# Performance work log

Measured on AMD Instinct MI355X. Metric: run time of the kernel, lower is better.

## Reference

```python
import jax, jax.numpy as jnp
import numpy as np

B, SRC_LEN, IN_DIM = 4096, 128, 16
H = 64
SEQ_LEN = 100
MEAN_DIM = 4
COV_DIM = MEAN_DIM + MEAN_DIM * (MEAN_DIM - 1) // 2  # 10
SKIP = 4


def _lin_init(key, out_d, in_d):
    k1, k2 = jax.random.split(key)
    bound = 1.0 / np.sqrt(in_d)
    W = jax.random.uniform(k1, (out_d, in_d), minval=-bound, maxval=bound, dtype=jnp.float32)
    b = jax.random.uniform(k2, (out_d,), minval=-bound, maxval=bound, dtype=jnp.float32)
    return W, b


def setup_inputs() -> dict:
    key = jax.random.key(0)
    ks = jax.random.split(key, 16)
    inp = {}
    inp["x"] = jax.random.normal(ks[0], (B, SRC_LEN, IN_DIM), dtype=jnp.float32)
    inp["trg"] = jax.random.normal(ks[1], (B, 1, SKIP), dtype=jnp.float32)
    # encoder GRU (1 layer)
    inp["enc_Wih"], inp["enc_bih"] = _lin_init(ks[2], 3 * H, IN_DIM)
    inp["enc_Whh"], inp["enc_bhh"] = _lin_init(ks[3], 3 * H, H)
    # decoder GRU (1 layer)
    inp["dec_Wih"], inp["dec_bih"] = _lin_init(ks[4], 3 * H, IN_DIM)
    inp["dec_Whh"], inp["dec_bhh"] = _lin_init(ks[5], 3 * H, H)
    # decoder.out: Linear(H -> IN_DIM)
    inp["out_W"], inp["out_b"] = _lin_init(ks[6], IN_DIM, H)
    # initEmbed: Linear(SKIP -> IN_DIM)
    inp["emb_W"], inp["emb_b"] = _lin_init(ks[7], IN_DIM, SKIP)
    # mean head: Linear(IN_DIM->H), GELU, Linear(H->MEAN_DIM)
    inp["mh_W1"], inp["mh_b1"] = _lin_init(ks[8], H, IN_DIM)
    inp["mh_W2"], inp["mh_b2"] = _lin_init(ks[9], MEAN_DIM, H)
    # cov head: Linear(IN_DIM->H), GELU, Linear(H->COV_DIM)
    inp["ch_W1"], inp["ch_b1"] = _lin_init(ks[10], H, IN_DIM)
    inp["ch_W2"], inp["ch_b2"] = _lin_init(ks[11], COV_DIM, H)
    return inp


def _gru_cell(h, xt, Wih, Whh, bih, bhh):
    # PyTorch GRU cell math. h, xt: [B, H], [B, in]
    gi = xt @ Wih.T + bih           # [B, 3H]
    gh = h @ Whh.T + bhh            # [B, 3H]
    i_r, i_z, i_n = jnp.split(gi, 3, axis=-1)
    h_r, h_z, h_n = jnp.split(gh, 3, axis=-1)
    r = jax.nn.sigmoid(i_r + h_r)
    z = jax.nn.sigmoid(i_z + h_z)
    n = jnp.tanh(i_n + r * h_n)
    return (1.0 - z) * n + z * h


def reference(x, trg, enc_Wih, enc_bih, enc_Whh, enc_bhh,
              dec_Wih, dec_bih, dec_Whh, dec_bhh,
              out_W, out_b, emb_W, emb_b,
              mh_W1, mh_b1, mh_W2, mh_b2,
              ch_W1, ch_b1, ch_W2, ch_b2):
    b = x.shape[0]
    # ---- encoder GRU over src_len; only final hidden is used downstream ----
    h0 = jnp.zeros((b, H), dtype=x.dtype)

    def enc_step(h, xt):
        h = _gru_cell(h, xt, enc_Wih, enc_Whh, enc_bih, enc_bhh)
        return h, None

    enc_h, _ = jax.lax.scan(enc_step, h0, jnp.swapaxes(x, 0, 1))

    init_in = trg[:, 0, :] @ emb_W.T + emb_b  # [B, IN_DIM]

    def dec_step(carry, _):
        h, inp = carry
        h = _gru_cell(h, inp, dec_Wih, dec_Whh, dec_bih, dec_bhh)
        o = h @ out_W.T + out_b               # [B, IN_DIM]
        nxt = jax.lax.stop_gradient(o)        # .detach() on fed-back input
        return (h, nxt), o

    (_, _), outs = jax.lax.scan(dec_step, (enc_h, init_in), None, length=SEQ_LEN)
    dec_out = jnp.swapaxes(outs, 0, 1)        # [B, SEQ_LEN, IN_DIM]

    # ---- output heads (Dropout is identity in eval) ----
    means = jax.nn.gelu(dec_out @ mh_W1.T + mh_b1, approximate=False) @ mh_W2.T + mh_b2
    covs = jax.nn.gelu(dec_out @ ch_W1.T + ch_b1, approximate=False) @ ch_W2.T + ch_b2

    inf = jnp.inf
    lower = jnp.array([-inf, -inf, -1.0, -1.0], dtype=means.dtype)
    upper = jnp.array([inf, inf, 1.0, 1.0], dtype=means.dtype)
    means = jnp.maximum(jnp.minimum(means, upper), lower)
    return means, covs
```

## Files before the change

### kernel.cpp

```cpp
#include <hip/hip_runtime.h>
#include <cstdint>
#include <cstddef>

#define BTOT    4096
#define SRCLEN  128
#define INDIM   16
#define HDIM    64
#define SEQLEN  100
#define MEANS_N (BTOT * SEQLEN * 4)

__device__ __forceinline__ float sigmoidf_(float x) {
    return __builtin_amdgcn_rcpf(1.0f + __expf(-x));
}
__device__ __forceinline__ float tanhf_(float x) {
    float e = __expf(2.0f * x);
    return 1.0f - 2.0f * __builtin_amdgcn_rcpf(e + 1.0f);
}
__device__ __forceinline__ float gelu_fast(float x) {
    float z = fabsf(x) * 0.70710678118654752440f;
    float t = __builtin_amdgcn_rcpf(1.0f + 0.3275911f * z);
    float p = t * (0.254829592f +
              t * (-0.284496736f +
              t * (1.421413741f +
              t * (-1.453152027f +
              t * 1.061405429f))));
    float er = 1.0f - p * __expf(-z * z);
    er = copysignf(er, x);
    return 0.5f * x * (1.0f + er);
}

typedef __attribute__((ext_vector_type(8))) short s8v;
typedef __attribute__((ext_vector_type(4))) float f4v;

__device__ __forceinline__ unsigned short f2bf(float x) {
    unsigned u = __float_as_uint(x);
    unsigned r = (u + 0x7FFFu + ((u >> 16) & 1u)) >> 16;
    return (unsigned short)r;
}
__device__ __forceinline__ float bf2f(unsigned short b) {
    return __uint_as_float(((unsigned)b) << 16);
}
__device__ __forceinline__ void split2(float4 a, float4 b, s8v& hi, s8v& lo) {
    float v[8] = {a.x, a.y, a.z, a.w, b.x, b.y, b.z, b.w};
    #pragma unroll
    for (int j = 0; j < 8; ++j) {
        unsigned short h = f2bf(v[j]);
        hi[j] = (short)h;
        lo[j] = (short)f2bf(v[j] - bf2f(h));
    }
}
__device__ __forceinline__ void split8(const float* v, s8v& hi, s8v& lo) {
    #pragma unroll
    for (int j = 0; j < 8; ++j) {
        unsigned short h = f2bf(v[j]);
        hi[j] = (short)h;
        lo[j] = (short)f2bf(v[j] - bf2f(h));
    }
}
__device__ __forceinline__ void load_bfrag(const float* p, s8v& hi, s8v& lo) {
    float4 a = *(const float4*)p;
    float4 b = *(const float4*)(p + 4);
    split2(a, b, hi, lo);
}

typedef __attribute__((ext_vector_type(2))) unsigned int u2v;
__device__ __forceinline__ float half_merge(float own_lo, float send_hi) {
    u2v r = __builtin_amdgcn_permlane32_swap(__float_as_uint(own_lo),
                                             __float_as_uint(send_hi),
                                             false, false);
    return __uint_as_float(r[0]);
}

#define MFMA16(a, b, c) __builtin_amdgcn_mfma_f32_16x16x32_bf16((a), (b), (c), 0, 0, 0)

__global__ __launch_bounds__(256, 2) void fused_gru_kernel(
    const float* __restrict__ x,
    const float* __restrict__ eWih, const float* __restrict__ ebih,
    const float* __restrict__ eWhh, const float* __restrict__ ebhh,
    const float* __restrict__ dWih, const float* __restrict__ dbih,
    const float* __restrict__ dWhh, const float* __restrict__ dbhh,
    const float* __restrict__ outW, const float* __restrict__ outb,
    const float* __restrict__ embW, const float* __restrict__ embb,
    const float* __restrict__ trg,
    float* __restrict__ dec_o)
{
    const int tid  = threadIdx.x;
    const int lane = tid & 63;
    const int w    = tid >> 6;
    const int col  = lane & 15;
    const int q    = lane >> 4;
    const int u    = w * 16 + col;
    const int b0   = blockIdx.x * 8;
    const int rj0  = (q & 1) * 4 + ((q >> 1) << 1);

    __shared__ __align__(16) unsigned short hiL[2][16][72];
    __shared__ __align__(16) unsigned short loL[2][16][72];
    __shared__ __align__(16) unsigned short xhi_l[64][9][16];
    __shared__ __align__(16) unsigned short xlo_l[64][9][16];
    __shared__ float outW_l[16][64];
    __shared__ float init_l[8][16];

    for (int i = tid; i < 16 * 64; i += 256) outW_l[i >> 6][i & 63] = outW[i];
    if (tid < 128) {
        int b = tid >> 4, jj = tid & 15;
        float s = embb[jj];
        #pragma unroll
        for (int s4 = 0; s4 < 4; ++s4)
            s = fmaf(embW[jj * 4 + s4], trg[(size_t)(b0 + b) * 4 + s4], s);
        init_l[b][jj] = s;
    }

    for (int i = tid; i < 2 * 16 * 72; i += 256) {
        ((unsigned short*)hiL)[i] = 0;
        ((unsigned short*)loL)[i] = 0;
    }
    for (int i = tid; i < 64 * 16; i += 256) {
        xhi_l[i >> 4][8][i & 15] = 0;
        xlo_l[i >> 4][8][i & 15] = 0;
    }

    auto stage_x = [&](int c) {
        #pragma unroll
        for (int k = 0; k < 8; ++k) {
            int f   = tid + k * 256;
            int b   = f >> 8;
            int rem = f & 255;
            int tl  = rem >> 2;
            int d4  = (rem & 3) << 2;
            const float* xp = x + ((size_t)(b0 + b) * SRCLEN + (c * 64 + tl)) * INDIM + d4;
            float4 v = *(const float4*)xp;
            float vv[4] = {v.x, v.y, v.z, v.w};
            unsigned short hh[4], ll[4];
            #pragma unroll
            for (int j = 0; j < 4; ++j) {
                hh[j] = f2bf(vv[j]);
                ll[j] = f2bf(vv[j] - bf2f(hh[j]));
            }
            *(ushort4*)&xhi_l[tl][b][d4] = make_ushort4(hh[0], hh[1], hh[2], hh[3]);
            *(ushort4*)&xlo_l[tl][b][d4] = make_ushort4(ll[0], ll[1], ll[2], ll[3]);
        }
    };

    const s8v z8 = {0, 0, 0, 0, 0, 0, 0, 0};
    const f4v z4 = {0.0f, 0.0f, 0.0f, 0.0f};

    {
        s8v brh[3], brl[3], bzh[3], bzl[3], bnhh[2], bnhl[2], bnxh, bnxl;
        load_bfrag(eWhh + (size_t)u * 64 + q * 8,              brh[0], brl[0]);
        load_bfrag(eWhh + (size_t)u * 64 + 32 + q * 8,         brh[1], brl[1]);
        load_bfrag(eWhh + (size_t)(64 + u) * 64 + q * 8,       bzh[0], bzl[0]);
        load_bfrag(eWhh + (size_t)(64 + u) * 64 + 32 + q * 8,  bzh[1], bzl[1]);
        load_bfrag(eWhh + (size_t)(128 + u) * 64 + q * 8,      bnhh[0], bnhl[0]);
        load_bfrag(eWhh + (size_t)(128 + u) * 64 + 32 + q * 8, bnhh[1], bnhl[1]);
        if (q < 2) {
            load_bfrag(eWih + (size_t)u * 16 + q * 8,         brh[2], brl[2]);
            load_bfrag(eWih + (size_t)(64 + u) * 16 + q * 8,  bzh[2], bzl[2]);
            load_bfrag(eWih + (size_t)(128 + u) * 16 + q * 8, bnxh, bnxl);
        } else {
            brh[2] = z8; brl[2] = z8; bzh[2] = z8; bzl[2] = z8; bnxh = z8; bnxl = z8;
        }

        const float br   = ebih[u] + ebhh[u];
        const float bz   = ebih[u + 64] + ebhh[u + 64];
        const float bnx  = ebih[u + 128];
        const float bnh  = ebhh[u + 128];

        const int xb   = (q < 2) ? (col & 7) : 8;
        const int xoff = (q & 1) * 8;
        const unsigned short* xh_base = &xhi_l[0][xb][xoff];
        const unsigned short* xl_base = &xlo_l[0][xb][xoff];

        stage_x(0);
        float hold2e[2] = {0.0f, 0.0f};
        __syncthreads();

        int cur = 0;
        for (int t = 0; t < SRCLEN; ++t) {
            if (t == 64) {
                stage_x(1);
                __syncthreads();
            }
            const int tl = t & 63;

            const s8v xh = *(const s8v*)(xh_base + (size_t)tl * 144);
            const s8v xl = *(const s8v*)(xl_base + (size_t)tl * 144);

            const s8v ah0 = *(const s8v*)&hiL[cur][col][q * 8];
            const s8v al0 = *(const s8v*)&loL[cur][col][q * 8];
            const s8v ah1 = *(const s8v*)&hiL[cur][col][32 + q * 8];
            const s8v al1 = *(const s8v*)&loL[cur][col][32 + q * 8];

            f4v accr, accz, accnh, accnx;
            accr  = MFMA16(ah0, brh[0], z4);
            accz  = MFMA16(ah0, bzh[0], z4);
            accnh = MFMA16(ah0, bnhh[0], z4);
            accr  = MFMA16(ah0, brl[0], accr);
            accz  = MFMA16(ah0, bzl[0], accz);
            accnh = MFMA16(ah0, bnhl[0], accnh);
            accr  = MFMA16(al0, brh[0], accr);
            accz  = MFMA16(al0, bzh[0], accz);
            accnh = MFMA16(al0, bnhh[0], accnh);
            accr  = MFMA16(ah1, brh[1], accr);
            accz  = MFMA16(ah1, bzh[1], accz);
            accnh = MFMA16(ah1, bnhh[1], accnh);
            accr  = MFMA16(ah1, brl[1], accr);
            accz  = MFMA16(ah1, bzl[1], accz);
            accnh = MFMA16(ah1, bnhl[1], accnh);
            accr  = MFMA16(al1, brh[1], accr);
            accz  = MFMA16(al1, bzh[1], accz);
            accnh = MFMA16(al1, bnhh[1], accnh);
            accr  = MFMA16(xh, brh[2], accr);
            accz  = MFMA16(xh, bzh[2], accz);
            accnx = MFMA16(xh, bnxh, z4);
            accr  = MFMA16(xh, brl[2], accr);
            accz  = MFMA16(xh, bzl[2], accz);
            accnx = MFMA16(xh, bnxl, accnx);
            accr  = MFMA16(xl, brh[2], accr);
            accz  = MFMA16(xl, bzh[2], accz);
            accnx = MFMA16(xl, bnxh, accnx);

            float pr[2], pz[2], pnh[2], pnx[2];
            pr[0]  = half_merge(accr[0],  accr[2]);
            pr[1]  = half_merge(accr[1],  accr[3]);
            pz[0]  = half_merge(accz[0],  accz[2]);
            pz[1]  = half_merge(accz[1],  accz[3]);
            pnh[0] = half_merge(accnh[0], accnh[2]);
            pnh[1] = half_merge(accnh[1], accnh[3]);
            pnx[0] = half_merge(accnx[0], accnx[2]);
            pnx[1] = half_merge(accnx[1], accnx[3]);

            const int nxt = cur ^ 1;
            #pragma unroll
            for (int j = 0; j < 2; ++j) {
                float r  = sigmoidf_(pr[j] + br);
                float zz = sigmoidf_(pz[j] + bz);
                float n  = tanhf_(pnx[j] + bnx + r * (pnh[j] + bnh));
                float h  = (1.0f - zz) * n + zz * hold2e[j];
                hold2e[j] = h;
                unsigned short hh = f2bf(h);
                hiL[nxt][rj0 + j][u] = hh;
                loL[nxt][rj0 + j][u] = f2bf(h - bf2f(hh));
            }
            __syncthreads();
            cur ^= 1;
        }

        float hold2[2] = {hold2e[0], hold2e[1]};

        float wh_r[16], wh_z[16], wh_n[16];
        #pragma unroll
        for (int c = 0; c < 2; ++c)
            #pragma unroll
            for (int jj = 0; jj < 8; ++jj) {
                int k = c * 32 + q * 8 + jj;
                wh_r[c * 8 + jj] = dWhh[(size_t)u * 64 + k];
                wh_z[c * 8 + jj] = dWhh[(size_t)(64 + u) * 64 + k];
                wh_n[c * 8 + jj] = dWhh[(size_t)(128 + u) * 64 + k];
            }
        float wi_r[16], wi_z[16], wi_n[16];
        #pragma unroll
        for (int j = 0; j < 16; ++j) {
            wi_r[j] = dWih[(size_t)u * 16 + j];
            wi_z[j] = dWih[(size_t)(64 + u) * 16 + j];
            wi_n[j] = dWih[(size_t)(128 + u) * 16 + j];
        }

        float m_r[16], m_z[16], c_in[16];
        #pragma unroll
        for (int c = 0; c < 2; ++c)
            #pragma unroll
            for (int jj = 0; jj < 8; ++jj) {
                int k = c * 32 + q * 8 + jj;
                float sr = 0.0f, sz = 0.0f, sn = 0.0f;
                #pragma unroll
                for (int j = 0; j < 16; ++j) {
                    float ow = outW_l[j][k];
                    sr = fmaf(wi_r[j], ow, sr);
                    sz = fmaf(wi_z[j], ow, sz);
                    sn = fmaf(wi_n[j], ow, sn);
                }
                m_r[c * 8 + jj]  = wh_r[c * 8 + jj] + sr;
                m_z[c * 8 + jj]  = wh_z[c * 8 + jj] + sz;
                c_in[c * 8 + jj] = sn;
            }

        s8v mrh[2], mrl[2], mzh[2], mzl[2], cinh[2], cinl[2], hnh[2], hnl[2];
        split8(m_r,      mrh[0],  mrl[0]);  split8(m_r + 8,  mrh[1],  mrl[1]);
        split8(m_z,      mzh[0],  mzl[0]);  split8(m_z + 8,  mzh[1],  mzl[1]);
        split8(c_in,     cinh[0], cinl[0]); split8(c_in + 8, cinh[1], cinl[1]);
        split8(wh_n,     hnh[0],  hnl[0]);  split8(wh_n + 8, hnh[1],  hnl[1]);
        s8v r0h[2], r0l[2], z0h[2], z0l[2];
        split8(wh_r, r0h[0], r0l[0]); split8(wh_r + 8, r0h[1], r0l[1]);
        split8(wh_z, z0h[0], z0l[0]); split8(wh_z + 8, z0h[1], z0l[1]);
        s8v owh[2], owl[2];
        {
            float ov[16];
            #pragma unroll
            for (int c = 0; c < 2; ++c)
                #pragma unroll
                for (int jj = 0; jj < 8; ++jj)
                    ov[c * 8 + jj] = outW_l[col][c * 32 + q * 8 + jj];
            split8(ov, owh[0], owl[0]); split8(ov + 8, owh[1], owl[1]);
        }

        float b_r = dbhh[u] + dbih[u];
        float b_z = dbhh[u + 64] + dbih[u + 64];
        float b_in = dbih[u + 128];
        const float b_hn = dbhh[u + 128];
        #pragma unroll
        for (int j = 0; j < 16; ++j) {
            float obj = outb[j];
            b_r  = fmaf(obj, wi_r[j], b_r);
            b_z  = fmaf(obj, wi_z[j], b_z);
            b_in = fmaf(obj, wi_n[j], b_in);
        }
        const float ob = outb[col];

        float g_r[2], g_z[2], g_n[2];
        #pragma unroll
        for (int j2 = 0; j2 < 2; ++j2) {
            int row = rj0 + j2;
            float sr = dbih[u] + dbhh[u];
            float sz = dbih[u + 64] + dbhh[u + 64];
            float sn = dbih[u + 128];
            #pragma unroll
            for (int j = 0; j < 16; ++j) {
                float iv = init_l[row][j];
                sr = fmaf(wi_r[j], iv, sr);
                sz = fmaf(wi_z[j], iv, sz);
                sn = fmaf(wi_n[j], iv, sn);
            }
            g_r[j2] = sr; g_z[j2] = sz; g_n[j2] = sn;
        }

        {
            const s8v ah0 = *(const s8v*)&hiL[0][col][q * 8];
            const s8v al0 = *(const s8v*)&loL[0][col][q * 8];
            const s8v ah1 = *(const s8v*)&hiL[0][col][32 + q * 8];
            const s8v al1 = *(const s8v*)&loL[0][col][32 + q * 8];
            f4v ar, az, ahn;
            ar  = MFMA16(ah0, r0h[0], z4);
            az  = MFMA16(ah0, z0h[0], z4);
            ahn = MFMA16(ah0, hnh[0], z4);
            ar  = MFMA16(ah0, r0l[0], ar);
            az  = MFMA16(ah0, z0l[0], az);
            ahn = MFMA16(ah0, hnl[0], ahn);
            ar  = MFMA16(al0, r0h[0], ar);
            az  = MFMA16(al0, z0h[0], az);
            ahn = MFMA16(al0, hnh[0], ahn);
            ar  = MFMA16(ah1, r0h[1], ar);
            az  = MFMA16(ah1, z0h[1], az);
            ahn = MFMA16(ah1, hnh[1], ahn);
            ar  = MFMA16(ah1, r0l[1], ar);
            az  = MFMA16(ah1, z0l[1], az);
            ahn = MFMA16(ah1, hnl[1], ahn);
            ar  = MFMA16(al1, r0h[1], ar);
            az  = MFMA16(al1, z0h[1], az);
            ahn = MFMA16(al1, hnh[1], ahn);

            float pr[2], pz[2], pnh[2];
            pr[0]  = half_merge(ar[0],  ar[2]);
            pr[1]  = half_merge(ar[1],  ar[3]);
            pz[0]  = half_merge(az[0],  az[2]);
            pz[1]  = half_merge(az[1],  az[3]);
            pnh[0] = half_merge(ahn[0], ahn[2]);
            pnh[1] = half_merge(ahn[1], ahn[3]);

            #pragma unroll
            for (int j = 0; j < 2; ++j) {
                float r  = sigmoidf_(pr[j] + g_r[j]);
                float zz = sigmoidf_(pz[j] + g_z[j]);
                float n  = tanhf_(g_n[j] + r * (pnh[j] + b_hn));
                float h  = (1.0f - zz) * n + zz * hold2[j];
                hold2[j] = h;
                unsigned short hh = f2bf(h);
                hiL[1][rj0 + j][u] = hh;
                loL[1][rj0 + j][u] = f2bf(h - bf2f(hh));
            }
            __syncthreads();
        }

        for (int t = 1; t < SEQLEN; ++t) {
            const int dcur = t & 1;
            const s8v ah0 = *(const s8v*)&hiL[dcur][col][q * 8];
            const s8v al0 = *(const s8v*)&loL[dcur][col][q * 8];
            const s8v ah1 = *(const s8v*)&hiL[dcur][col][32 + q * 8];
            const s8v al1 = *(const s8v*)&loL[dcur][col][32 + q * 8];

            if (w == ((t - 1) & 3)) {
                f4v oa;
                oa = MFMA16(ah0, owh[0], z4);
                oa = MFMA16(ah0, owl[0], oa);
                oa = MFMA16(al0, owh[0], oa);
                oa = MFMA16(ah1, owh[1], oa);
                oa = MFMA16(ah1, owl[1], oa);
                oa = MFMA16(al1, owh[1], oa);
                if (q < 2) {
                    #pragma unroll
                    for (int i = 0; i < 4; ++i)
                        dec_o[(((size_t)(b0 + q * 4 + i) * SEQLEN) + (t - 1)) * INDIM + col] = oa[i] + ob;
                }
            }

            f4v ar, az, ain, ahn;
            ar  = MFMA16(ah0, mrh[0], z4);
            az  = MFMA16(ah0, mzh[0], z4);
            ain = MFMA16(ah0, cinh[0], z4);
            ahn = MFMA16(ah0, hnh[0], z4);
            ar  = MFMA16(ah0, mrl[0], ar);
            az  = MFMA16(ah0, mzl[0], az);
            ain = MFMA16(ah0, cinl[0], ain);
            ahn = MFMA16(ah0, hnl[0], ahn);
            ar  = MFMA16(al0, mrh[0], ar);
            az  = MFMA16(al0, mzh[0], az);
            ain = MFMA16(al0, cinh[0], ain);
            ahn = MFMA16(al0, hnh[0], ahn);
            ar  = MFMA16(ah1, mrh[1], ar);
            az  = MFMA16(ah1, mzh[1], az);
            ain = MFMA16(ah1, cinh[1], ain);
            ahn = MFMA16(ah1, hnh[1], ahn);
            ar  = MFMA16(ah1, mrl[1], ar);
            az  = MFMA16(ah1, mzl[1], az);
            ain = MFMA16(ah1, cinl[1], ain);
            ahn = MFMA16(ah1, hnl[1], ahn);
            ar  = MFMA16(al1, mrh[1], ar);
            az  = MFMA16(al1, mzh[1], az);
            ain = MFMA16(al1, cinh[1], ain);
            ahn = MFMA16(al1, hnh[1], ahn);

            float pr[2], pz[2], pin[2], pnh[2];
            pr[0]  = half_merge(ar[0],  ar[2]);
            pr[1]  = half_merge(ar[1],  ar[3]);
            pz[0]  = half_merge(az[0],  az[2]);
            pz[1]  = half_merge(az[1],  az[3]);
            pin[0] = half_merge(ain[0], ain[2]);
            pin[1] = half_merge(ain[1], ain[3]);
            pnh[0] = half_merge(ahn[0], ahn[2]);
            pnh[1] = half_merge(ahn[1], ahn[3]);

            const int nxt = dcur ^ 1;
            #pragma unroll
            for (int j = 0; j < 2; ++j) {
                float r  = sigmoidf_(pr[j] + b_r);
                float zz = sigmoidf_(pz[j] + b_z);
                float n  = tanhf_(pin[j] + b_in + r * (pnh[j] + b_hn));
                float h  = (1.0f - zz) * n + zz * hold2[j];
                hold2[j] = h;
                unsigned short hh = f2bf(h);
                hiL[nxt][rj0 + j][u] = hh;
                loL[nxt][rj0 + j][u] = f2bf(h - bf2f(hh));
            }
            __syncthreads();
        }

        if (w == 0) {
            const s8v ah0 = *(const s8v*)&hiL[0][col][q * 8];
            const s8v al0 = *(const s8v*)&loL[0][col][q * 8];
            const s8v ah1 = *(const s8v*)&hiL[0][col][32 + q * 8];
            const s8v al1 = *(const s8v*)&loL[0][col][32 + q * 8];
            f4v oa;
            oa = MFMA16(ah0, owh[0], z4);
            oa = MFMA16(ah0, owl[0], oa);
            oa = MFMA16(al0, owh[0], oa);
            oa = MFMA16(ah1, owh[1], oa);
            oa = MFMA16(ah1, owl[1], oa);
            oa = MFMA16(al1, owh[1], oa);
            if (q < 2) {
                #pragma unroll
                for (int i = 0; i < 4; ++i)
                    dec_o[(((size_t)(b0 + q * 4 + i) * SEQLEN) + (SEQLEN - 1)) * INDIM + col] = oa[i] + ob;
            }
        }
    }
}

__global__ __launch_bounds__(256) void heads_mfma_kernel(
    const float* __restrict__ dec_o,
    const float* __restrict__ mW1, const float* __restrict__ mb1,
    const float* __restrict__ mW2, const float* __restrict__ mb2,
    const float* __restrict__ cW1, const float* __restrict__ cb1,
    const float* __restrict__ cW2, const float* __restrict__ cb2,
    float* __restrict__ out)
{
    const int tid  = threadIdx.x;
    const int lane = tid & 63;
    const int w    = tid >> 6;
    const int col  = lane & 15;
    const int q    = lane >> 4;

    __shared__ __align__(16) unsigned short Hm_hi[4][16][72];
    __shared__ __align__(16) unsigned short Hm_lo[4][16][72];
    __shared__ __align__(16) unsigned short Hc_hi[4][16][72];
    __shared__ __align__(16) unsigned short Hc_lo[4][16][72];

    const s8v z8 = {0, 0, 0, 0, 0, 0, 0, 0};
    const f4v z4 = {0.0f, 0.0f, 0.0f, 0.0f};

    s8v w1mh[4], w1ml[4], w1ch[4], w1cl[4];
    #pragma unroll
    for (int c = 0; c < 4; ++c) {
        if (q < 2) {
            load_bfrag(mW1 + (size_t)(c * 16 + col) * 16 + q * 8, w1mh[c], w1ml[c]);
            load_bfrag(cW1 + (size_t)(c * 16 + col) * 16 + q * 8, w1ch[c], w1cl[c]);
        } else {
            w1mh[c] = z8; w1ml[c] = z8; w1ch[c] = z8; w1cl[c] = z8;
        }
    }
    s8v w2mh[2], w2ml[2], w2ch[2], w2cl[2];
    if (col < 4) {
        load_bfrag(mW2 + (size_t)col * 64 + q * 8,      w2mh[0], w2ml[0]);
        load_bfrag(mW2 + (size_t)col * 64 + 32 + q * 8, w2mh[1], w2ml[1]);
    } else {
        w2mh[0] = z8; w2ml[0] = z8; w2mh[1] = z8; w2ml[1] = z8;
    }
    if (col < 10) {
        load_bfrag(cW2 + (size_t)col * 64 + q * 8,      w2ch[0], w2cl[0]);
        load_bfrag(cW2 + (size_t)col * 64 + 32 + q * 8, w2ch[1], w2cl[1]);
    } else {
        w2ch[0] = z8; w2cl[0] = z8; w2ch[1] = z8; w2cl[1] = z8;
    }

    float b1m[4], b1c[4];
    #pragma unroll
    for (int c = 0; c < 4; ++c) {
        b1m[c] = mb1[c * 16 + col];
        b1c[c] = cb1[c * 16 + col];
    }
    const float b2m = (col < 4)  ? mb2[col] : 0.0f;
    const float b2c = (col < 10) ? cb2[col] : 0.0f;

    float* means = out;
    float* covs  = out + MEANS_N;

    const int wave_id = blockIdx.x * 4 + w;

    #pragma unroll 1
    for (int it = 0; it < 4; ++it) {
        const int tile = wave_id + 6400 * it;
        const size_t r0 = (size_t)tile * 16;

        s8v ah, al;
        if (q < 2) {
            load_bfrag(dec_o + (r0 + (size_t)col) * 16 + q * 8, ah, al);
        } else { ah = z8; al = z8; }

        #pragma unroll
        for (int c = 0; c < 4; ++c) {
            f4v am = MFMA16(ah, w1mh[c], z4);
            am = MFMA16(ah, w1ml[c], am);
            am = MFMA16(al, w1mh[c], am);
            f4v ac = MFMA16(ah, w1ch[c], z4);
            ac = MFMA16(ah, w1cl[c], ac);
            ac = MFMA16(al, w1ch[c], ac);
            #pragma unroll
            for (int i = 0; i < 4; ++i) {
                float hm = gelu_fast(am[i] + b1m[c]);
                unsigned short hh = f2bf(hm);
                Hm_hi[w][q * 4 + i][c * 16 + col] = hh;
                Hm_lo[w][q * 4 + i][c * 16 + col] = f2bf(hm - bf2f(hh));
                float hc = gelu_fast(ac[i] + b1c[c]);
                hh = f2bf(hc);
                Hc_hi[w][q * 4 + i][c * 16 + col] = hh;
                Hc_lo[w][q * 4 + i][c * 16 + col] = f2bf(hc - bf2f(hh));
            }
        }

        const s8v amh0 = *(const s8v*)&Hm_hi[w][col][q * 8];
        const s8v amh1 = *(const s8v*)&Hm_hi[w][col][32 + q * 8];
        const s8v aml0 = *(const s8v*)&Hm_lo[w][col][q * 8];
        const s8v aml1 = *(const s8v*)&Hm_lo[w][col][32 + q * 8];
        const s8v ach0 = *(const s8v*)&Hc_hi[w][col][q * 8];
        const s8v ach1 = *(const s8v*)&Hc_hi[w][col][32 + q * 8];
        const s8v acl0 = *(const s8v*)&Hc_lo[w][col][q * 8];
        const s8v acl1 = *(const s8v*)&Hc_lo[w][col][32 + q * 8];

        f4v om, oc;
        om = MFMA16(amh0, w2mh[0], z4);
        om = MFMA16(amh0, w2ml[0], om);
        om = MFMA16(aml0, w2mh[0], om);
        om = MFMA16(amh1, w2mh[1], om);
        om = MFMA16(amh1, w2ml[1], om);
        om = MFMA16(aml1, w2mh[1], om);
        oc = MFMA16(ach0, w2ch[0], z4);
        oc = MFMA16(ach0, w2cl[0], oc);
        oc = MFMA16(acl0, w2ch[0], oc);
        oc = MFMA16(ach1, w2ch[1], oc);
        oc = MFMA16(ach1, w2cl[1], oc);
        oc = MFMA16(acl1, w2ch[1], oc);

        if (col < 4) {
            #pragma unroll
            for (int i = 0; i < 4; ++i) {
                float v = om[i] + b2m;
                if (col >= 2) v = fminf(fmaxf(v, -1.0f), 1.0f);
                means[(r0 + q * 4 + i) * 4 + col] = v;
            }
        }
        if (col < 10) {
            #pragma unroll
            for (int i = 0; i < 4; ++i)
                covs[(r0 + q * 4 + i) * 10 + col] = oc[i] + b2c;
        }
    }
}

extern "C" void kernel_launch(void* const* d_in, const int* in_sizes, int n_in,
                              void* d_out, int out_size, void* d_ws, size_t ws_size,
                              hipStream_t stream)
{
    const float* x    = (const float*)d_in[0];
    const float* trg  = (const float*)d_in[1];
    const float* eWih = (const float*)d_in[2];
    const float* ebih = (const float*)d_in[3];
    const float* eWhh = (const float*)d_in[4];
    const float* ebhh = (const float*)d_in[5];
    const float* dWih = (const float*)d_in[6];
    const float* dbih = (const float*)d_in[7];
    const float* dWhh = (const float*)d_in[8];
    const float* dbhh = (const float*)d_in[9];
    const float* outW = (const float*)d_in[10];
    const float* outb = (const float*)d_in[11];
    const float* embW = (const float*)d_in[12];
    const float* embb = (const float*)d_in[13];
    const float* mW1  = (const float*)d_in[14];
    const float* mb1  = (const float*)d_in[15];
    const float* mW2  = (const float*)d_in[16];
    const float* mb2  = (const float*)d_in[17];
    const float* cW1  = (const float*)d_in[18];
    const float* cb1  = (const float*)d_in[19];
    const float* cW2  = (const float*)d_in[20];
    const float* cb2  = (const float*)d_in[21];

    float* ws    = (float*)d_ws;
    float* dec_o = ws;
    float* outp  = (float*)d_out;

    fused_gru_kernel<<<dim3(BTOT / 8), dim3(256), 0, stream>>>(
        x, eWih, ebih, eWhh, ebhh, dWih, dbih, dWhh, dbhh,
        outW, outb, embW, embb, trg, dec_o);
    heads_mfma_kernel<<<dim3(1600), dim3(256), 0, stream>>>(
        dec_o, mW1, mb1, mW2, mb2, cW1, cb1, cW2, cb2, outp);
}
```

Before: 349.0 us.

## Fuse output heads into decoder loop as a software-pipelined stage

Removes the separate heads kernel and the dec_o workspace round trip. The heads now run inside the decoder time loop: the per-step output goes to shared memory, layer 1 of both heads runs one step later, and layer 2 runs two steps later on waves 2 and 3. This saves a kernel launch and the global write and read of the decoder outputs, hiding head work in the latency-bound recurrence. In exchange it adds MFMA and GELU work, two extra loop iterations, and more shared memory and registers in a kernel launched with launch_bounds(256,2).

After: 477.3 us. 36.8% more time.

```diff
diff --git a/kernel.cpp b/kernel.cpp
--- a/kernel.cpp
+++ b/kernel.cpp
@@ -82,7 +82,11 @@
     const float* __restrict__ outW, const float* __restrict__ outb,
     const float* __restrict__ embW, const float* __restrict__ embb,
     const float* __restrict__ trg,
-    float* __restrict__ dec_o)
+    const float* __restrict__ mW1, const float* __restrict__ mb1,
+    const float* __restrict__ mW2, const float* __restrict__ mb2,
+    const float* __restrict__ cW1, const float* __restrict__ cb1,
+    const float* __restrict__ cW2, const float* __restrict__ cb2,
+    float* __restrict__ out)
 {
     const int tid  = threadIdx.x;
     const int lane = tid & 63;
@@ -99,6 +103,11 @@
     __shared__ __align__(16) unsigned short xlo_l[64][9][16];
     __shared__ float outW_l[16][64];
     __shared__ float init_l[8][16];
+    __shared__ __align__(16) float o_sl[2][8][16];
+    __shared__ __align__(16) unsigned short Hm_hi[2][8][72];
+    __shared__ __align__(16) unsigned short Hm_lo[2][8][72];
+    __shared__ __align__(16) unsigned short Hc_hi[2][8][72];
+    __shared__ __align__(16) unsigned short Hc_lo[2][8][72];
 
     for (int i = tid; i < 16 * 64; i += 256) outW_l[i >> 6][i & 63] = outW[i];
     if (tid < 128) {
@@ -144,6 +153,7 @@
     const s8v z8 = {0, 0, 0, 0, 0, 0, 0, 0};
     const f4v z4 = {0.0f, 0.0f, 0.0f, 0.0f};
 
+    float hold2e[2];
     {
         s8v brh[3], brl[3], bzh[3], bzl[3], bnhh[2], bnhl[2], bnxh, bnxl;
         load_bfrag(eWhh + (size_t)u * 64 + q * 8,              brh[0], brl[0]);
@@ -171,7 +181,7 @@
         const unsigned short* xl_base = &xlo_l[0][xb][xoff];
 
         stage_x(0);
-        float hold2e[2] = {0.0f, 0.0f};
+        hold2e[0] = 0.0f; hold2e[1] = 0.0f;
         __syncthreads();
 
         int cur = 0;
@@ -244,7 +254,9 @@
             __syncthreads();
             cur ^= 1;
         }
-
+    }
+
+    {
         float hold2[2] = {hold2e[0], hold2e[1]};
 
         float wh_r[16], wh_z[16], wh_n[16];
@@ -315,6 +327,33 @@
             b_in = fmaf(obj, wi_n[j], b_in);
         }
         const float ob = outb[col];
+
+        s8v w1mh, w1ml, w1ch, w1cl;
+        if (q < 2) {
+            load_bfrag(mW1 + (size_t)(w * 16 + col) * 16 + q * 8, w1mh, w1ml);
+            load_bfrag(cW1 + (size_t)(w * 16 + col) * 16 + q * 8, w1ch, w1cl);
+        } else { w1mh = z8; w1ml = z8; w1ch = z8; w1cl = z8; }
+        const float b1m = mb1[w * 16 + col];
+        const float b1c = cb1[w * 16 + col];
+        s8v w2h[2], w2l[2];
+        w2h[0] = z8; w2l[0] = z8; w2h[1] = z8; w2l[1] = z8;
+        float b2 = 0.0f;
+        if (w == 2) {
+            if (col < 4) {
+                load_bfrag(mW2 + (size_t)col * 64 + q * 8,      w2h[0], w2l[0]);
+                load_bfrag(mW2 + (size_t)col * 64 + 32 + q * 8, w2h[1], w2l[1]);
+                b2 = mb2[col];
+            }
+        } else if (w == 3) {
+            if (col < 10) {
+                load_bfrag(cW2 + (size_t)col * 64 + q * 8,      w2h[0], w2l[0]);
+                load_bfrag(cW2 + (size_t)col * 64 + 32 + q * 8, w2h[1], w2l[1]);
+                b2 = cb2[col];
+            }
+        }
+
+        float* means = out;
+        float* covs  = out + MEANS_N;
 
         float g_r[2], g_z[2], g_n[2];
         #pragma unroll
@@ -380,226 +419,161 @@
             __syncthreads();
         }
 
-        for (int t = 1; t < SEQLEN; ++t) {
+        for (int t = 1; t <= SEQLEN + 2; ++t) {
             const int dcur = t & 1;
-            const s8v ah0 = *(const s8v*)&hiL[dcur][col][q * 8];
-            const s8v al0 = *(const s8v*)&loL[dcur][col][q * 8];
-            const s8v ah1 = *(const s8v*)&hiL[dcur][col][32 + q * 8];
-            const s8v al1 = *(const s8v*)&loL[dcur][col][32 + q * 8];
-
-            if (w == ((t - 1) & 3)) {
-                f4v oa;
-                oa = MFMA16(ah0, owh[0], z4);
-                oa = MFMA16(ah0, owl[0], oa);
-                oa = MFMA16(al0, owh[0], oa);
-                oa = MFMA16(ah1, owh[1], oa);
-                oa = MFMA16(ah1, owl[1], oa);
-                oa = MFMA16(al1, owh[1], oa);
+
+            if (t <= SEQLEN) {
+                const s8v ah0 = *(const s8v*)&hiL[dcur][col][q * 8];
+                const s8v al0 = *(const s8v*)&loL[dcur][col][q * 8];
+                const s8v ah1 = *(const s8v*)&hiL[dcur][col][32 + q * 8];
+                const s8v al1 = *(const s8v*)&loL[dcur][col][32 + q * 8];
+
+                if (w == ((t - 1) & 3)) {
+                    f4v oa;
+                    oa = MFMA16(ah0, owh[0], z4);
+                    oa = MFMA16(ah0, owl[0], oa);
+                    oa = MFMA16(al0, owh[0], oa);
+                    oa = MFMA16(ah1, owh[1], oa);
+                    oa = MFMA16(ah1, owl[1], oa);
+                    oa = MFMA16(al1, owh[1], oa);
+                    if (q < 2) {
+                        #pragma unroll
+                        for (int i = 0; i < 4; ++i)
+                            o_sl[dcur][q * 4 + i][col] = oa[i] + ob;
+                    }
+                }
+
+                if (t < SEQLEN) {
+                    f4v ar, az, ain, ahn;
+                    ar  = MFMA16(ah0, mrh[0], z4);
+                    az  = MFMA16(ah0, mzh[0], z4);
+                    ain = MFMA16(ah0, cinh[0], z4);
+                    ahn = MFMA16(ah0, hnh[0], z4);
+                    ar  = MFMA16(ah0, mrl[0], ar);
+                    az  = MFMA16(ah0, mzl[0], az);
+                    ain = MFMA16(ah0, cinl[0], ain);
+                    ahn = MFMA16(ah0, hnl[0], ahn);
+                    ar  = MFMA16(al0, mrh[0], ar);
+                    az  = MFMA16(al0, mzh[0], az);
+                    ain = MFMA16(al0, cinh[0], ain);
+                    ahn = MFMA16(al0, hnh[0], ahn);
+                    ar  = MFMA16(ah1, mrh[1], ar);
+                    az  = MFMA16(ah1, mzh[1], az);
+                    ain = MFMA16(ah1, cinh[1], ain);
+                    ahn = MFMA16(ah1, hnh[1], ahn);
+                    ar  = MFMA16(ah1, mrl[1], ar);
+                    az  = MFMA16(ah1, mzl[1], az);
+                    ain = MFMA16(ah1, cinl[1], ain);
+                    ahn = MFMA16(ah1, hnl[1], ahn);
+                    ar  = MFMA16(al1, mrh[1], ar);
+                    az  = MFMA16(al1, mzh[1], az);
+                    ain = MFMA16(al1, cinh[1], ain);
+                    ahn = MFMA16(al1, hnh[1], ahn);
+
+                    float pr[2], pz[2], pin[2], pnh[2];
+                    pr[0]  = half_merge(ar[0],  ar[2]);
+                    pr[1]  = half_merge(ar[1],  ar[3]);
+                    pz[0]  = half_merge(az[0],  az[2]);
+                    pz[1]  = half_merge(az[1],  az[3]);
+                    pin[0] = half_merge(ain[0], ain[2]);
+                    pin[1] = half_merge(ain[1], ain[3]);
+                    pnh[0] = half_merge(ahn[0], ahn[2]);
+                    pnh[1] = half_merge(ahn[1], ahn[3]);
+
+                    const int nxt = dcur ^ 1;
+                    #pragma unroll
+                    for (int j = 0; j < 2; ++j) {
+                        float r  = sigmoidf_(pr[j] + b_r);
+                        float zz = sigmoidf_(pz[j] + b_z);
+                        float n  = tanhf_(pin[j] + b_in + r * (pnh[j] + b_hn));
+                        float h  = (1.0f - zz) * n + zz * hold2[j];
+                        hold2[j] = h;
+                        unsigned short hh = f2bf(h);
+                        hiL[nxt][rj0 + j][u] = hh;
+                        loL[nxt][rj0 + j][u] = f2bf(h - bf2f(hh));
+                    }
+                }
+            }
+
+            if (t >= 2) {
+                const int po = (t - 1) & 1;
+                const int ph = t & 1;
+                s8v aoh, aol;
+                if (q < 2 && col < 8) {
+                    float4 a = *(const float4*)&o_sl[po][col][q * 8];
+                    float4 b = *(const float4*)&o_sl[po][col][q * 8 + 4];
+                    split2(a, b, aoh, aol);
+                } else { aoh = z8; aol = z8; }
+
+                f4v am = MFMA16(aoh, w1mh, z4);
+                am = MFMA16(aoh, w1ml, am);
+                am = MFMA16(aol, w1mh, am);
+                f4v ac = MFMA16(aoh, w1ch, z4);
+                ac = MFMA16(aoh, w1cl, ac);
+                ac = MFMA16(aol, w1ch, ac);
+
                 if (q < 2) {
                     #pragma unroll
-                    for (int i = 0; i < 4; ++i)
-                        dec_o[(((size_t)(b0 + q * 4 + i) * SEQLEN) + (t - 1)) * INDIM + col] = oa[i] + ob;
+                    for (int i = 0; i < 4; ++i) {
+                        float hm = gelu_fast(am[i] + b1m);
+                        unsigned short hh = f2bf(hm);
+                        Hm_hi[ph][q * 4 + i][w * 16 + col] = hh;
+                        Hm_lo[ph][q * 4 + i][w * 16 + col] = f2bf(hm - bf2f(hh));
+                        float hc = gelu_fast(ac[i] + b1c);
+                        hh = f2bf(hc);
+                        Hc_hi[ph][q * 4 + i][w * 16 + col] = hh;
+                        Hc_lo[ph][q * 4 + i][w * 16 + col] = f2bf(hc - bf2f(hh));
+                    }
                 }
             }
 
-            f4v ar, az, ain, ahn;
-            ar  = MFMA16(ah0, mrh[0], z4);
-            az  = MFMA16(ah0, mzh[0], z4);
-            ain = MFMA16(ah0, cinh[0], z4);
-            ahn = MFMA16(ah0, hnh[0], z4);
-            ar  = MFMA16(ah0, mrl[0], ar);
-            az  = MFMA16(ah0, mzl[0], az);
-            ain = MFMA16(ah0, cinl[0], ain);
-            ahn = MFMA16(ah0, hnl[0], ahn);
-            ar  = MFMA16(al0, mrh[0], ar);
-            az  = MFMA16(al0, mzh[0], az);
-            ain = MFMA16(al0, cinh[0], ain);
-            ahn = MFMA16(al0, hnh[0], ahn);
-            ar  = MFMA16(ah1, mrh[1], ar);
-            az  = MFMA16(ah1, mzh[1], az);
-            ain = MFMA16(ah1, cinh[1], ain);
-            ahn = MFMA16(ah1, hnh[1], ahn);
-            ar  = MFMA16(ah1, mrl[1], ar);
-            az  = MFMA16(ah1, mzl[1], az);
-            ain = MFMA16(ah1, cinl[1], ain);
-            ahn = MFMA16(ah1, hnl[1], ahn);
-            ar  = MFMA16(al1, mrh[1], ar);
-            az  = MFMA16(al1, mzh[1], az);
-            ain = MFMA16(al1, cinh[1], ain);
-            ahn = MFMA16(al1, hnh[1], ahn);
-
-            float pr[2], pz[2], pin[2], pnh[2];
-            pr[0]  = half_merge(ar[0],  ar[2]);
-            pr[1]  = half_merge(ar[1],  ar[3]);
-            pz[0]  = half_merge(az[0],  az[2]);
-            pz[1]  = half_merge(az[1],  az[3]);
-            pin[0] = half_merge(ain[0], ain[2]);
-            pin[1] = half_merge(ain[1], ain[3]);
-            pnh[0] = half_merge(ahn[0], ahn[2]);
-            pnh[1] = half_merge(ahn[1], ahn[3]);
-
-            const int nxt = dcur ^ 1;
-            #pragma unroll
-            for (int j = 0; j < 2; ++j) {
-                float r  = sigmoidf_(pr[j] + b_r);
-                float zz = sigmoidf_(pz[j] + b_z);
-                float n  = tanhf_(pin[j] + b_in + r * (pnh[j] + b_hn));
-                float h  = (1.0f - zz) * n + zz * hold2[j];
-                hold2[j] = h;
-                unsigned short hh = f2bf(h);
-                hiL[nxt][rj0 + j][u] = hh;
-                loL[nxt][rj0 + j][u] = f2bf(h - bf2f(hh));
-            }
+            if (t >= 3 && w >= 2) {
+                const int ph2 = (t - 1) & 1;
+                const int step = t - 3;
+                s8v a0h, a0l, a1h, a1l;
+                if (col < 8) {
+                    if (w == 2) {
+                        a0h = *(const s8v*)&Hm_hi[ph2][col][q * 8];
+                        a0l = *(const s8v*)&Hm_lo[ph2][col][q * 8];
+                        a1h = *(const s8v*)&Hm_hi[ph2][col][32 + q * 8];
+                        a1l = *(const s8v*)&Hm_lo[ph2][col][32 + q * 8];
+                    } else {
+                        a0h = *(const s8v*)&Hc_hi[ph2][col][q * 8];
+                        a0l = *(const s8v*)&Hc_lo[ph2][col][q * 8];
+                        a1h = *(const s8v*)&Hc_hi[ph2][col][32 + q * 8];
+                        a1l = *(const s8v*)&Hc_lo[ph2][col][32 + q * 8];
+                    }
+                } else { a0h = z8; a0l = z8; a1h = z8; a1l = z8; }
+
+                f4v o2;
+                o2 = MFMA16(a0h, w2h[0], z4);
+                o2 = MFMA16(a0h, w2l[0], o2);
+                o2 = MFMA16(a0l, w2h[0], o2);
+                o2 = MFMA16(a1h, w2h[1], o2);
+                o2 = MFMA16(a1h, w2l[1], o2);
+                o2 = MFMA16(a1l, w2h[1], o2);
+
+                if (q < 2) {
+                    if (w == 2) {
+                        if (col < 4) {
+                            #pragma unroll
+                            for (int i = 0; i < 4; ++i) {
+                                float v = o2[i] + b2;
+                                if (col >= 2) v = fminf(fmaxf(v, -1.0f), 1.0f);
+                                means[(((size_t)(b0 + q * 4 + i) * SEQLEN) + step) * 4 + col] = v;
+                            }
+                        }
+                    } else {
+                        if (col < 10) {
+                            #pragma unroll
+                            for (int i = 0; i < 4; ++i)
+                                covs[(((size_t)(b0 + q * 4 + i) * SEQLEN) + step) * 10 + col] = o2[i] + b2;
+                        }
+                    }
+                }
+            }
+
             __syncthreads();
-        }
-
-        if (w == 0) {
-            const s8v ah0 = *(const s8v*)&hiL[0][col][q * 8];
-            const s8v al0 = *(const s8v*)&loL[0][col][q * 8];
-            const s8v ah1 = *(const s8v*)&hiL[0][col][32 + q * 8];
-            const s8v al1 = *(const s8v*)&loL[0][col][32 + q * 8];
-            f4v oa;
-            oa = MFMA16(ah0, owh[0], z4);
-            oa = MFMA16(ah0, owl[0], oa);
-            oa = MFMA16(al0, owh[0], oa);
-            oa = MFMA16(ah1, owh[1], oa);
-            oa = MFMA16(ah1, owl[1], oa);
-            oa = MFMA16(al1, owh[1], oa);
-            if (q < 2) {
-                #pragma unroll
-                for (int i = 0; i < 4; ++i)
-                    dec_o[(((size_t)(b0 + q * 4 + i) * SEQLEN) + (SEQLEN - 1)) * INDIM + col] = oa[i] + ob;
-            }
-        }
-    }
-}
-
-__global__ __launch_bounds__(256) void heads_mfma_kernel(
-    const float* __restrict__ dec_o,
-    const float* __restrict__ mW1, const float* __restrict__ mb1,
-    const float* __restrict__ mW2, const float* __restrict__ mb2,
-    const float* __restrict__ cW1, const float* __restrict__ cb1,
-    const float* __restrict__ cW2, const float* __restrict__ cb2,
-    float* __restrict__ out)
-{
-    const int tid  = threadIdx.x;
-    const int lane = tid & 63;
-    const int w    = tid >> 6;
-    const int col  = lane & 15;
-    const int q    = lane >> 4;
-
-    __shared__ __align__(16) unsigned short Hm_hi[4][16][72];
-    __shared__ __align__(16) unsigned short Hm_lo[4][16][72];
-    __shared__ __align__(16) unsigned short Hc_hi[4][16][72];
-    __shared__ __align__(16) unsigned short Hc_lo[4][16][72];
-
-    const s8v z8 = {0, 0, 0, 0, 0, 0, 0, 0};
-    const f4v z4 = {0.0f, 0.0f, 0.0f, 0.0f};
-
-    s8v w1mh[4], w1ml[4], w1ch[4], w1cl[4];
-    #pragma unroll
-    for (int c = 0; c < 4; ++c) {
-        if (q < 2) {
-            load_bfrag(mW1 + (size_t)(c * 16 + col) * 16 + q * 8, w1mh[c], w1ml[c]);
-            load_bfrag(cW1 + (size_t)(c * 16 + col) * 16 + q * 8, w1ch[c], w1cl[c]);
-        } else {
-            w1mh[c] = z8; w1ml[c] = z8; w1ch[c] = z8; w1cl[c] = z8;
-        }
-    }
-    s8v w2mh[2], w2ml[2], w2ch[2], w2cl[2];
-    if (col < 4) {
-        load_bfrag(mW2 + (size_t)col * 64 + q * 8,      w2mh[0], w2ml[0]);
-        load_bfrag(mW2 + (size_t)col * 64 + 32 + q * 8, w2mh[1], w2ml[1]);
-    } else {
-        w2mh[0] = z8; w2ml[0] = z8; w2mh[1] = z8; w2ml[1] = z8;
-    }
-    if (col < 10) {
-        load_bfrag(cW2 + (size_t)col * 64 + q * 8,      w2ch[0], w2cl[0]);
-        load_bfrag(cW2 + (size_t)col * 64 + 32 + q * 8, w2ch[1], w2cl[1]);
-    } else {
-        w2ch[0] = z8; w2cl[0] = z8; w2ch[1] = z8; w2cl[1] = z8;
-    }
-
-    float b1m[4], b1c[4];
-    #pragma unroll
-    for (int c = 0; c < 4; ++c) {
-        b1m[c] = mb1[c * 16 + col];
-        b1c[c] = cb1[c * 16 + col];
-    }
-    const float b2m = (col < 4)  ? mb2[col] : 0.0f;
-    const float b2c = (col < 10) ? cb2[col] : 0.0f;
-
-    float* means = out;
-    float* covs  = out + MEANS_N;
-
-    const int wave_id = blockIdx.x * 4 + w;
-
-    #pragma unroll 1
-    for (int it = 0; it < 4; ++it) {
-        const int tile = wave_id + 6400 * it;
-        const size_t r0 = (size_t)tile * 16;
-
-        s8v ah, al;
-        if (q < 2) {
-            load_bfrag(dec_o + (r0 + (size_t)col) * 16 + q * 8, ah, al);
-        } else { ah = z8; al = z8; }
-
-        #pragma unroll
-        for (int c = 0; c < 4; ++c) {
-            f4v am = MFMA16(ah, w1mh[c], z4);
-            am = MFMA16(ah, w1ml[c], am);
-            am = MFMA16(al, w1mh[c], am);
-            f4v ac = MFMA16(ah, w1ch[c], z4);
-            ac = MFMA16(ah, w1cl[c], ac);
-            ac = MFMA16(al, w1ch[c], ac);
-            #pragma unroll
-            for (int i = 0; i < 4; ++i) {
-                float hm = gelu_fast(am[i] + b1m[c]);
-                unsigned short hh = f2bf(hm);
-                Hm_hi[w][q * 4 + i][c * 16 + col] = hh;
-                Hm_lo[w][q * 4 + i][c * 16 + col] = f2bf(hm - bf2f(hh));
-                float hc = gelu_fast(ac[i] + b1c[c]);
-                hh = f2bf(hc);
-                Hc_hi[w][q * 4 + i][c * 16 + col] = hh;
-                Hc_lo[w][q * 4 + i][c * 16 + col] = f2bf(hc - bf2f(hh));
-            }
-        }
-
-        const s8v amh0 = *(const s8v*)&Hm_hi[w][col][q * 8];
-        const s8v amh1 = *(const s8v*)&Hm_hi[w][col][32 + q * 8];
-        const s8v aml0 = *(const s8v*)&Hm_lo[w][col][q * 8];
-        const s8v aml1 = *(const s8v*)&Hm_lo[w][col][32 + q * 8];
-        const s8v ach0 = *(const s8v*)&Hc_hi[w][col][q * 8];
-        const s8v ach1 = *(const s8v*)&Hc_hi[w][col][32 + q * 8];
-        const s8v acl0 = *(const s8v*)&Hc_lo[w][col][q * 8];
-        const s8v acl1 = *(const s8v*)&Hc_lo[w][col][32 + q * 8];
-
-        f4v om, oc;
-        om = MFMA16(amh0, w2mh[0], z4);
-        om = MFMA16(amh0, w2ml[0], om);
-        om = MFMA16(aml0, w2mh[0], om);
-        om = MFMA16(amh1, w2mh[1], om);
-        om = MFMA16(amh1, w2ml[1], om);
-        om = MFMA16(aml1, w2mh[1], om);
-        oc = MFMA16(ach0, w2ch[0], z4);
-        oc = MFMA16(ach0, w2cl[0], oc);
-        oc = MFMA16(acl0, w2ch[0], oc);
-        oc = MFMA16(ach1, w2ch[1], oc);
-        oc = MFMA16(ach1, w2cl[1], oc);
-        oc = MFMA16(acl1, w2ch[1], oc);
-
-        if (col < 4) {
-            #pragma unroll
-            for (int i = 0; i < 4; ++i) {
-                float v = om[i] + b2m;
-                if (col >= 2) v = fminf(fmaxf(v, -1.0f), 1.0f);
-                means[(r0 + q * 4 + i) * 4 + col] = v;
-            }
-        }
-        if (col < 10) {
-            #pragma unroll
-            for (int i = 0; i < 4; ++i)
-                covs[(r0 + q * 4 + i) * 10 + col] = oc[i] + b2c;
         }
     }
 }
@@ -631,13 +605,10 @@
     const float* cW2  = (const float*)d_in[20];
     const float* cb2  = (const float*)d_in[21];
 
-    float* ws    = (float*)d_ws;
-    float* dec_o = ws;
-    float* outp  = (float*)d_out;
+    float* outp = (float*)d_out;
 
     fused_gru_kernel<<<dim3(BTOT / 8), dim3(256), 0, stream>>>(
         x, eWih, ebih, eWhh, ebhh, dWih, dbih, dWhh, dbhh,
-        outW, outb, embW, embb, trg, dec_o);
-    heads_mfma_kernel<<<dim3(1600), dim3(256), 0, stream>>>(
-        dec_o, mW1, mb1, mW2, mb2, cW1, cb1, cW2, cb2, outp);
-}
+        outW, outb, embW, embb, trg,
+        mW1, mb1, mW2, mb2, cW1, cb1, cW2, cb2, outp);
+}
```
